# Kernel tuning notes

Measured on AMD Instinct MI355X. Metric: run time of the kernel, lower is better.

Reference implementation:

```python
import jax, jax.numpy as jnp
import numpy as np
import math

GAMMA = 0.97      # discounting
LAM = 0.95        # gae lambda
EPSILON = 0.3     # ppo clip
EPS = 0.2         # gpo clip (eps)
ENT_COST = 0.01
RSCALE = 1.0
ALPHA = 1.0
NUM_STEPS = 1.0e6 # normalization step count buffer


def _mlp(x, Ws, bs):
    for i, (W, b) in enumerate(zip(Ws, bs)):
        x = x @ W.T + b
        if i < len(Ws) - 1:
            x = jax.nn.silu(x)
    return x


def _dist_create(logits):
    loc, s = jnp.split(logits, 2, axis=-1)
    return loc, jax.nn.softplus(s) + 0.001


def _log_det_jac(x):
    # tanh bijector log|det J| per element
    return 2.0 * (math.log(2.0) - x - jax.nn.softplus(-2.0 * x))


def _log_prob(loc, scale, dist):
    lu = -0.5 * jnp.square((dist - loc) / scale)
    ln = 0.5 * math.log(2.0 * math.pi) + jnp.log(scale)
    return (lu - ln - _log_det_jac(dist)).sum(-1)


def _entropy(loc, scale, noise):
    ln = 0.5 * math.log(2.0 * math.pi) + jnp.log(scale)
    ent = (0.5 + ln) * jnp.ones_like(loc)
    dist = loc + scale * noise  # reparameterized sample (torch.normal)
    return (ent + _log_det_jac(dist)).sum(-1)


def _kl(pl, ps, ql, qs):
    vr = jnp.square(ps / qs)
    t1 = jnp.square((pl - ql) / qs)
    return (0.5 * (vr + t1 - 1.0 - jnp.log(vr))).mean(-1)


def _normalize(obs, rm, rv):
    var = jnp.clip(rv / (NUM_STEPS + 1.0), 1e-6, 1e6)
    return jnp.clip((obs - rm) / jnp.sqrt(var), -5.0, 5.0)


def _gae(truncation, termination, reward, values, bootstrap_value):
    tm = 1.0 - truncation
    v1 = jnp.concatenate([values[1:], bootstrap_value[None]], 0)
    deltas = (reward + GAMMA * (1.0 - termination) * v1 - values) * tm

    def step(acc, xs):
        d, te, tmask = xs
        acc = d + GAMMA * (1.0 - te) * tmask * LAM * acc
        return acc, acc

    _, vmx = jax.lax.scan(step, jnp.zeros_like(bootstrap_value),
                          (deltas, termination, tm), reverse=True)
    vs = vmx + values
    vs1 = jnp.concatenate([vs[1:], bootstrap_value[None]], 0)
    adv = (reward + GAMMA * (1.0 - termination) * vs1 - values) * tm
    return vs, adv


def _loss(observation, pobservation, reward, done, truncation, logits, action,
          noise, pw0, pb0, pw1, pb1, pw2, pb2, vw0, vb0, vw1, vb1, vw2, vb2,
          running_mean, running_variance, kl_coef):
    sg = jax.lax.stop_gradient
    Pw, Pb = [pw0, pw1, pw2], [pb0, pb1, pb2]
    Vw, Vb = [vw0, vw1, vw2], [vb0, vb1, vb2]

    obs_n = _normalize(observation, running_mean, running_variance)
    pobs_n = _normalize(pobservation, running_mean, running_variance)

    guider_logits = _mlp(obs_n[:-1], Pw, Pb)
    learner_logits = _mlp(pobs_n[:-1], Pw, Pb)
    baseline = _mlp(obs_n, Vw, Vb).squeeze(-1)  # [T+1, B]
    bootstrap = baseline[-1]
    baseline = baseline[:-1]

    reward_s = reward * RSCALE
    termination = done * (1.0 - truncation)

    loc, scale = _dist_create(logits)
    b_lp = _log_prob(loc, scale, action)
    gl, gs = _dist_create(guider_logits)
    g_lp = _log_prob(gl, gs, action)
    ll, ls = _dist_create(learner_logits)
    l_lp = _log_prob(ll, ls, action)

    kl_learner = _kl(sg(gl), sg(gs), ll, ls).mean()
    kl_guider = _kl(gl, gs, sg(ll), sg(ls))
    # use_clip = True branch
    diff = g_lp - l_lp
    m = jnp.where(diff > math.log(1.0 + EPS), 1.0,
                  jnp.where(diff < math.log(1.0 - EPS), 1.0, 0.0))
    kl_guider = (kl_guider * m).mean()

    vs, adv = _gae(truncation, termination, reward_s, sg(baseline), sg(bootstrap))
    vs = sg(vs)
    adv = sg((adv - adv.mean()) / (jnp.std(adv, ddof=1) + 1e-5))

    rho = jnp.exp(g_lp - b_lp)
    rho_clip = jnp.exp(jnp.clip(g_lp - sg(l_lp), math.log(1.0 - EPS), math.log(1.0 + EPS))
                       + sg(l_lp) - b_lp)
    rho_clip = jnp.clip(rho_clip, 1.0 - EPSILON, 1.0 + EPSILON)
    guider_policy_loss = -jnp.mean(jnp.minimum(rho * adv, rho_clip * adv))

    rho2 = jnp.exp(jnp.minimum(l_lp - b_lp, 10.0))  # stable_exp
    rho2c = jnp.clip(rho2, 1.0 - EPSILON, 1.0 + EPSILON)
    learner_policy_loss = -jnp.mean(jnp.minimum(rho2 * adv, rho2c * adv))

    v_err = vs - baseline
    v_loss = jnp.mean(v_err * v_err) * 0.25

    entropy = jnp.mean(_entropy(loc, scale, noise))
    entropy_loss = -ENT_COST * entropy

    learner_loss = kl_learner + learner_policy_loss * ALPHA  # use_clip
    guider_loss = kl_guider + guider_policy_loss
    total = learner_loss + guider_loss + v_loss + entropy_loss
    return total, guider_loss, learner_loss, kl_learner


def setup_inputs() -> dict:
    key = jax.random.key(0)
    T, B, OBS, ACT, H = 1024, 256, 64, 8, 256
    ks = iter(jax.random.split(key, 32))

    def lin(fin, fout):
        W = jax.random.normal(next(ks), (fout, fin), jnp.float32) / np.float32(np.sqrt(fin))
        b = jnp.zeros((fout,), jnp.float32)
        return W, b

    pw0, pb0 = lin(OBS, H); pw1, pb1 = lin(H, H); pw2, pb2 = lin(H, 2 * ACT)
    vw0, vb0 = lin(OBS, H); vw1, vb1 = lin(H, H); vw2, vb2 = lin(H, 1)

    observation = jax.random.normal(next(ks), (T + 1, B, OBS), jnp.float32)
    pobservation = observation + 0.1 * jax.random.normal(next(ks), (T + 1, B, OBS), jnp.float32)
    reward = jax.random.normal(next(ks), (T, B), jnp.float32)
    done = (jax.random.uniform(next(ks), (T, B)) < 0.01).astype(jnp.float32)
    truncation = (jax.random.uniform(next(ks), (T, B)) < 0.005).astype(jnp.float32)
    logits = 0.5 * jax.random.normal(next(ks), (T, B, 2 * ACT), jnp.float32)
    action = jax.random.normal(next(ks), (T, B, ACT), jnp.float32)
    noise = jax.random.normal(next(ks), (T, B, ACT), jnp.float32)
    running_mean = jnp.zeros((OBS,), jnp.float32)
    running_variance = jnp.ones((OBS,), jnp.float32) * NUM_STEPS  # unit variance after /num_steps
    kl_coef = jnp.ones((1,), jnp.float32)

    return {"observation": observation, "pobservation": pobservation,
            "reward": reward, "done": done, "truncation": truncation,
            "logits": logits, "action": action, "noise": noise,
            "pw0": pw0, "pb0": pb0, "pw1": pw1, "pb1": pb1, "pw2": pw2, "pb2": pb2,
            "vw0": vw0, "vb0": vb0, "vw1": vw1, "vb1": vb1, "vw2": vw2, "vb2": vb2,
            "running_mean": running_mean, "running_variance": running_variance,
            "kl_coef": kl_coef}


def reference(observation, pobservation, reward, done, truncation, logits, action,
              noise, pw0, pb0, pw1, pb1, pw2, pb2, vw0, vb0, vw1, vb1, vw2, vb2,
              running_mean, running_variance, kl_coef):
    return _loss(observation, pobservation, reward, done, truncation, logits,
                 action, noise, pw0, pb0, pw1, pb1, pw2, pb2, vw0, vb0, vw1, vb1,
                 vw2, vb2, running_mean, running_variance, kl_coef)
```

## Files before the change

### kernel.cpp

```cpp
#include <hip/hip_runtime.h>
#include <math.h>

#define GAMMA_   0.97f
#define LAM_     0.95f
#define EPSILON_ 0.3f
#define HLOG2PI_ 0.91893853320467274f
#define LOG2C_   0.69314718055994531f
#define LOG1P2_  0.18232155679395463f
#define LOG0P8_  (-0.22314355131420976f)

typedef unsigned short u16;
typedef unsigned int   u32;
typedef _Float16 half8 __attribute__((ext_vector_type(8)));
typedef _Float16 half4 __attribute__((ext_vector_type(4)));
typedef __attribute__((ext_vector_type(4))) float floatx4;
typedef __attribute__((ext_vector_type(8))) float floatx8;

constexpr int  TT     = 1024;
constexpr long ROWS_P = (long)TT * 256;
constexpr long ROWS_V = (long)(TT + 1) * 256;

constexpr long FR_W0P_HI = 0;
constexpr long FR_W0P_LO = 16384;
constexpr long FR_W1P_HI = 32768;
constexpr long FR_W1P_LO = 98304;
constexpr long FR_W2P_HI = 163840;
constexpr long FR_W2P_LO = 167936;
constexpr long FR_W0V_HI = 172032;
constexpr long FR_W0V_LO = 188416;
constexpr long FR_W1V_HI = 204800;
constexpr long FR_W1V_LO = 270336;
constexpr long FR_W2V_HI = 335872;
constexpr long FR_W2V_LO = 339968;
constexpr long FR_TOTAL  = 344064;

constexpr long WS_ACC  = 0;
constexpr long WS_INV  = 32;
constexpr long WS_ADV  = 96;
constexpr long WS_BASE = WS_ADV + ROWS_P;
constexpr long WS_GA   = WS_BASE + ROWS_V;
constexpr long WS_GP   = WS_GA + 8192;
constexpr long WS_BANK = WS_GP + 8192;


__device__ __forceinline__ float softplus_f(float x) {
  return (x > 20.f) ? x : log1pf(expf(x));
}
__device__ __forceinline__ float silu_f(float x) {
  return x * __builtin_amdgcn_rcpf(1.f + __expf(-x));
}
__device__ __forceinline__ float clamp30(float x) {
  return fminf(1e30f, fmaxf(-1e30f, x));
}

__global__ void convert_kernel(const float* __restrict__ pw0,
                               const float* __restrict__ pw1,
                               const float* __restrict__ pw2,
                               const float* __restrict__ vw0,
                               const float* __restrict__ vw1,
                               const float* __restrict__ vw2,
                               const float* __restrict__ rv,
                               float* __restrict__ inv_std,
                               float* __restrict__ accum,
                               float* __restrict__ accumB,
                               u16* __restrict__ frag) {
  if (blockIdx.x == 0) {
    int t = threadIdx.x;
    if (t < 32) accum[t] = 0.f;
    for (int i = t; i < 1024; i += 256) accumB[i] = 0.f;
    if (t < 64) {
      float var = rv[t] / 1000001.0f;
      var = fminf(1e6f, fmaxf(1e-6f, var));
      inv_std[t] = 1.f / sqrtf(var);
    }
  }
  int idx = blockIdx.x * 256 + threadIdx.x;
  const float* W; int kslog, K, nvalid; long hioff, looff; int e;
  if (idx < 16384)       { W = pw0; e = idx;          kslog = 1; K = 64;  nvalid = 256; hioff = FR_W0P_HI; looff = FR_W0P_LO; }
  else if (idx < 81920)  { W = pw1; e = idx - 16384;  kslog = 3; K = 256; nvalid = 256; hioff = FR_W1P_HI; looff = FR_W1P_LO; }
  else if (idx < 86016)  { W = pw2; e = idx - 81920;  kslog = 3; K = 256; nvalid = 16;  hioff = FR_W2P_HI; looff = FR_W2P_LO; }
  else if (idx < 102400) { W = vw0; e = idx - 86016;  kslog = 1; K = 64;  nvalid = 256; hioff = FR_W0V_HI; looff = FR_W0V_LO; }
  else if (idx < 167936) { W = vw1; e = idx - 102400; kslog = 3; K = 256; nvalid = 256; hioff = FR_W1V_HI; looff = FR_W1V_LO; }
  else                   { W = vw2; e = idx - 167936; kslog = 3; K = 256; nvalid = 1;   hioff = FR_W2V_HI; looff = FR_W2V_LO; }
  int j    = e & 7;
  int lane = (e >> 3) & 63;
  int ks   = (e >> 9) & ((1 << kslog) - 1);
  int nt   = e >> (9 + kslog);
  int n = nt * 16 + (lane & 15);
  int k = ks * 32 + ((lane >> 4) << 3) + j;
  float w = (n < nvalid) ? W[n * K + k] : 0.f;
  _Float16 hi = (_Float16)w;
  _Float16 lo = (_Float16)(w - (float)hi);
  frag[hioff + e] = *(u16*)&hi;
  frag[looff + e] = *(u16*)&lo;
}

constexpr int SX = 72;
constexpr int SH = 264;
constexpr int SO = 20;

__global__ __launch_bounds__(256, 3)
void policy_kernel(const float* __restrict__ obs,
                   const float* __restrict__ pobs,
                   const float* __restrict__ rm,
                   const float* __restrict__ inv_std,
                   const u16* __restrict__ frag,
                   const float* __restrict__ b0,
                   const float* __restrict__ b1,
                   const float* __restrict__ b2,
                   const float* __restrict__ logits,
                   const float* __restrict__ action,
                   const float* __restrict__ noise,
                   const float* __restrict__ adv,
                   const float* __restrict__ accum,
                   float* __restrict__ accumB) {
  __shared__ __align__(16) _Float16 H[64 * SH];
  __shared__ __align__(16) float OUTT[64 * SO];
  __shared__ float red[160];

  const int tid  = threadIdx.x;
  const long row0 = (long)blockIdx.x * 32;
  const int lane = tid & 63;
  const int wv   = tid >> 6;
  const int lm   = lane & 15;
  const int lq   = lane >> 4;

  _Float16* X = H;

  #pragma unroll
  for (int it = 0; it < 2; ++it) {
    int flat = it * 256 + tid;
    int vr = flat >> 3;
    int f0 = (flat & 7) * 8;
    const float* src = (vr < 32) ? obs : pobs;
    floatx8 v  = *(const floatx8*)&src[(row0 + (vr & 31)) * 64 + f0];
    floatx8 m  = *(const floatx8*)&rm[f0];
    floatx8 is = *(const floatx8*)&inv_std[f0];
    half8 h;
    #pragma unroll
    for (int j = 0; j < 8; ++j)
      h[j] = (_Float16)fminf(5.f, fmaxf(-5.f, (v[j] - m[j]) * is[j]));
    *(half8*)&X[vr * SX + f0] = h;
  }

  const int  er   = tid >> 3;
  const int  ed   = tid & 7;
  const long erow = row0 + er;
  float pf_a   = action[erow * 8 + ed];
  float pf_loc = logits[erow * 16 + ed];
  float pf_sr  = logits[erow * 16 + 8 + ed];
  float pf_nd  = noise[erow * 8 + ed];
  float pf_adv = adv[erow];
  float pf_s3  = accum[3];
  float pf_s4  = accum[4];

  const half8* B0h = (const half8*)(frag + FR_W0P_HI);
  const half8* B0l = (const half8*)(frag + FR_W0P_LO);
  half8 B0hr[2][4], B0lr[2][4];
  #pragma unroll
  for (int ks = 0; ks < 2; ++ks)
    #pragma unroll
    for (int nt = 0; nt < 4; ++nt) {
      int ntg = wv * 4 + nt;
      B0hr[ks][nt] = B0h[(ntg * 2 + ks) * 64 + lane];
      B0lr[ks][nt] = B0l[(ntg * 2 + ks) * 64 + lane];
    }

  floatx4 acc[4][4];
  #pragma unroll
  for (int nt = 0; nt < 4; ++nt) {
    floatx4 bz = *(const floatx4*)&b0[(wv * 4 + nt) * 16 + lq * 4];
    #pragma unroll
    for (int mt = 0; mt < 4; ++mt) acc[mt][nt] = bz;
  }
  __syncthreads();

  #pragma unroll
  for (int ks = 0; ks < 2; ++ks) {
    half8 A[4];
    #pragma unroll
    for (int mt = 0; mt < 4; ++mt)
      A[mt] = *(const half8*)&X[(mt * 16 + lm) * SX + ks * 32 + lq * 8];
    __builtin_amdgcn_s_setprio(1);
    #pragma unroll
    for (int mt = 0; mt < 4; ++mt)
      #pragma unroll
      for (int nt = 0; nt < 4; ++nt)
        acc[mt][nt] = __builtin_amdgcn_mfma_f32_16x16x32_f16(B0hr[ks][nt], A[mt], acc[mt][nt], 0, 0, 0);
    #pragma unroll
    for (int mt = 0; mt < 4; ++mt)
      #pragma unroll
      for (int nt = 0; nt < 4; ++nt)
        acc[mt][nt] = __builtin_amdgcn_mfma_f32_16x16x32_f16(B0lr[ks][nt], A[mt], acc[mt][nt], 0, 0, 0);
    __builtin_amdgcn_s_setprio(0);
  }

  const half8* B1h = (const half8*)(frag + FR_W1P_HI);
  const half8* B1l = (const half8*)(frag + FR_W1P_LO);
  half8 Bh[4], Bl[4], Bhn[4], Bln[4];
  #pragma unroll
  for (int nt = 0; nt < 4; ++nt) {
    int ntg = wv * 4 + nt;
    Bh[nt] = B1h[(ntg * 8) * 64 + lane];
    Bl[nt] = B1l[(ntg * 8) * 64 + lane];
  }

  __syncthreads();
  #pragma unroll
  for (int nt = 0; nt < 4; ++nt) {
    int colbase = (wv * 4 + nt) * 16 + lq * 4;
    #pragma unroll
    for (int mt = 0; mt < 4; ++mt) {
      int row = mt * 16 + lm;
      half4 h;
      #pragma unroll
      for (int reg = 0; reg < 4; ++reg)
        h[reg] = (_Float16)silu_f(acc[mt][nt][reg]);
      *(half4*)&H[row * SH + colbase] = h;
    }
  }
  #pragma unroll
  for (int nt = 0; nt < 4; ++nt) {
    floatx4 bz = *(const floatx4*)&b1[(wv * 4 + nt) * 16 + lq * 4];
    #pragma unroll
    for (int mt = 0; mt < 4; ++mt) acc[mt][nt] = bz;
  }
  __syncthreads();

  #pragma unroll 1
  for (int ks = 0; ks < 8; ++ks) {
    if (ks < 7) {
      #pragma unroll
      for (int nt = 0; nt < 4; ++nt) {
        int ntg = wv * 4 + nt;
        Bhn[nt] = B1h[(ntg * 8 + ks + 1) * 64 + lane];
        Bln[nt] = B1l[(ntg * 8 + ks + 1) * 64 + lane];
      }
    }
    half8 A[4];
    #pragma unroll
    for (int mt = 0; mt < 4; ++mt)
      A[mt] = *(const half8*)&H[(mt * 16 + lm) * SH + ks * 32 + lq * 8];
    __builtin_amdgcn_s_setprio(1);
    #pragma unroll
    for (int mt = 0; mt < 4; ++mt)
      #pragma unroll
      for (int nt = 0; nt < 4; ++nt)
        acc[mt][nt] = __builtin_amdgcn_mfma_f32_16x16x32_f16(Bh[nt], A[mt], acc[mt][nt], 0, 0, 0);
    #pragma unroll
    for (int mt = 0; mt < 4; ++mt)
      #pragma unroll
      for (int nt = 0; nt < 4; ++nt)
        acc[mt][nt] = __builtin_amdgcn_mfma_f32_16x16x32_f16(Bl[nt], A[mt], acc[mt][nt], 0, 0, 0);
    __builtin_amdgcn_s_setprio(0);
    if (ks < 7) {
      #pragma unroll
      for (int nt = 0; nt < 4; ++nt) { Bh[nt] = Bhn[nt]; Bl[nt] = Bln[nt]; }
    }
  }

  const half8* B2h = (const half8*)(frag + FR_W2P_HI);
  const half8* B2l = (const half8*)(frag + FR_W2P_LO);
  half8 B2hr[8], B2lr[8];
  #pragma unroll
  for (int ks = 0; ks < 8; ++ks) {
    B2hr[ks] = B2h[ks * 64 + lane];
    B2lr[ks] = B2l[ks * 64 + lane];
  }

  __syncthreads();
  #pragma unroll
  for (int nt = 0; nt < 4; ++nt) {
    int colbase = (wv * 4 + nt) * 16 + lq * 4;
    #pragma unroll
    for (int mt = 0; mt < 4; ++mt) {
      int row = mt * 16 + lm;
      half4 h;
      #pragma unroll
      for (int reg = 0; reg < 4; ++reg)
        h[reg] = (_Float16)silu_f(acc[mt][nt][reg]);
      *(half4*)&H[row * SH + colbase] = h;
    }
  }
  __syncthreads();

  {
    floatx4 c3a = (floatx4){0.f,0.f,0.f,0.f};
    floatx4 c3b = (floatx4){0.f,0.f,0.f,0.f};
    __builtin_amdgcn_s_setprio(1);
    #pragma unroll
    for (int ks = 0; ks < 8; ks += 2) {
      half8 A0 = *(const half8*)&H[(wv * 16 + lm) * SH + ks * 32 + lq * 8];
      half8 A1 = *(const half8*)&H[(wv * 16 + lm) * SH + (ks + 1) * 32 + lq * 8];
      c3a = __builtin_amdgcn_mfma_f32_16x16x32_f16(B2hr[ks],     A0, c3a, 0, 0, 0);
      c3b = __builtin_amdgcn_mfma_f32_16x16x32_f16(B2hr[ks + 1], A1, c3b, 0, 0, 0);
      c3a = __builtin_amdgcn_mfma_f32_16x16x32_f16(B2lr[ks],     A0, c3a, 0, 0, 0);
      c3b = __builtin_amdgcn_mfma_f32_16x16x32_f16(B2lr[ks + 1], A1, c3b, 0, 0, 0);
    }
    __builtin_amdgcn_s_setprio(0);
    floatx4 bias = *(const floatx4*)&b2[lq * 4];
    floatx4 o = c3a + c3b + bias;
    #pragma unroll
    for (int reg = 0; reg < 4; ++reg)
      OUTT[(wv * 16 + lm) * SO + lq * 4 + reg] = o[reg];
  }
  __syncthreads();

  {
    int r = er;
    int d = ed;

    float gl  = OUTT[r * SO + d];
    float gsr = OUTT[r * SO + 8 + d];
    float ll  = OUTT[(32 + r) * SO + d];
    float lsr = OUTT[(32 + r) * SO + 8 + d];
    float a   = pf_a;
    float loc = pf_loc;
    float sr  = pf_sr;
    float nd  = pf_nd;

    float gs = softplus_f(gsr) + 1e-3f;
    float ls = softplus_f(lsr) + 1e-3f;
    float sc = softplus_f(sr) + 1e-3f;
    float ldj = 2.f * (LOG2C_ - a - softplus_f(-2.f * a));
    float lgs = logf(gs), lls = logf(ls), lsc = logf(sc);
    float zg = (a - gl) / gs;
    float zl = (a - ll) / ls;
    float z  = (a - loc) / sc;
    float glp = -0.5f * zg * zg - lgs - HLOG2PI_ - ldj;
    float llp = -0.5f * zl * zl - lls - HLOG2PI_ - ldj;
    float blp = -0.5f * z * z - lsc - HLOG2PI_ - ldj;
    float ratio = gs / ls;
    float vr = ratio * ratio;
    float t1 = (gl - ll) / ls; t1 *= t1;
    float kl = 0.5f * (vr + t1 - 1.f) - (lgs - lls);
    float dist = loc + sc * nd;
    float ent = 0.5f + HLOG2PI_ + lsc
              + 2.f * (LOG2C_ - dist - softplus_f(-2.f * dist));

    #pragma unroll
    for (int o = 4; o > 0; o >>= 1) {
      glp += __shfl_down(glp, o, 8);
      llp += __shfl_down(llp, o, 8);
      blp += __shfl_down(blp, o, 8);
      kl  += __shfl_down(kl, o, 8);
      ent += __shfl_down(ent, o, 8);
    }

    if (d == 0) {
      kl *= 0.125f;
      kl  = clamp30(kl);
      ent = clamp30(ent);

      float diff = glp - llp;
      float m = (diff > LOG1P2_ || diff < LOG0P8_) ? 1.f : 0.f;

      float N = (float)ROWS_P;
      float sum = pf_s3, sumsq = pf_s4;
      float mean = sum / N;
      float var  = fmaxf((sumsq - sum * sum / N) / (N - 1.f), 0.f);
      float inv  = 1.f / (sqrtf(var) + 1e-5f);
      float a_n  = (pf_adv - mean) * inv;

      float rho = expf(fminf(glp - blp, 80.f));
      float cl  = fminf(LOG1P2_, fmaxf(LOG0P8_, diff));
      float rc  = expf(fminf(cl + llp - blp, 80.f));
      rc = fminf(1.f + EPSILON_, fmaxf(1.f - EPSILON_, rc));
      float gp = clamp30(fminf(rho * a_n, rc * a_n));

      float rho2 = expf(fminf(llp - blp, 10.f));
      float r2c  = fminf(1.f + EPSILON_, fmaxf(1.f - EPSILON_, rho2));
      float lp = clamp30(fminf(rho2 * a_n, r2c * a_n));

      red[r]       = kl;
      red[32 + r]  = kl * m;
      red[64 + r]  = ent;
      red[96 + r]  = gp;
      red[128 + r] = lp;
    }
  }
  __syncthreads();
  if (tid < 32) {
    float s0 = red[tid], s1 = red[32 + tid], s2 = red[64 + tid];
    float s3 = red[96 + tid], s4 = red[128 + tid];
    #pragma unroll
    for (int o = 16; o > 0; o >>= 1) {
      s0 += __shfl_down(s0, o, 32);
      s1 += __shfl_down(s1, o, 32);
      s2 += __shfl_down(s2, o, 32);
      s3 += __shfl_down(s3, o, 32);
      s4 += __shfl_down(s4, o, 32);
    }
    if (tid == 0) {
      float* bank = accumB + (blockIdx.x & 31) * 32;
      atomicAdd(&bank[0], s0);
      atomicAdd(&bank[1], s1);
      atomicAdd(&bank[2], s2);
      atomicAdd(&bank[6], s3);
      atomicAdd(&bank[7], s4);
    }
  }
}

__global__ __launch_bounds__(256, 3)
void value_kernel(const float* __restrict__ obs,
                  const float* __restrict__ rm,
                  const float* __restrict__ inv_std,
                  const u16* __restrict__ frag,
                  const float* __restrict__ b0,
                  const float* __restrict__ b1,
                  const float* __restrict__ b2,
                  float* __restrict__ baseline) {
  __shared__ __align__(16) _Float16 H[64 * SH];

  const int tid  = threadIdx.x;
  const long row0 = (long)blockIdx.x * 64;
  const int lane = tid & 63;
  const int wv   = tid >> 6;
  const int lm   = lane & 15;
  const int lq   = lane >> 4;

  _Float16* X = H;

  #pragma unroll
  for (int it = 0; it < 2; ++it) {
    int flat = it * 256 + tid;
    int vr = flat >> 3;
    int f0 = (flat & 7) * 8;
    floatx8 v  = *(const floatx8*)&obs[(row0 + vr) * 64 + f0];
    floatx8 m  = *(const floatx8*)&rm[f0];
    floatx8 is = *(const floatx8*)&inv_std[f0];
    half8 h;
    #pragma unroll
    for (int j = 0; j < 8; ++j)
      h[j] = (_Float16)fminf(5.f, fmaxf(-5.f, (v[j] - m[j]) * is[j]));
    *(half8*)&X[vr * SX + f0] = h;
  }

  const half8* B0h = (const half8*)(frag + FR_W0V_HI);
  const half8* B0l = (const half8*)(frag + FR_W0V_LO);
  half8 B0hr[2][4], B0lr[2][4];
  #pragma unroll
  for (int ks = 0; ks < 2; ++ks)
    #pragma unroll
    for (int nt = 0; nt < 4; ++nt) {
      int ntg = wv * 4 + nt;
      B0hr[ks][nt] = B0h[(ntg * 2 + ks) * 64 + lane];
      B0lr[ks][nt] = B0l[(ntg * 2 + ks) * 64 + lane];
    }

  floatx4 acc[4][4];
  #pragma unroll
  for (int nt = 0; nt < 4; ++nt) {
    floatx4 bz = *(const floatx4*)&b0[(wv * 4 + nt) * 16 + lq * 4];
    #pragma unroll
    for (int mt = 0; mt < 4; ++mt) acc[mt][nt] = bz;
  }
  __syncthreads();

  #pragma unroll
  for (int ks = 0; ks < 2; ++ks) {
    half8 A[4];
    #pragma unroll
    for (int mt = 0; mt < 4; ++mt)
      A[mt] = *(const half8*)&X[(mt * 16 + lm) * SX + ks * 32 + lq * 8];
    __builtin_amdgcn_s_setprio(1);
    #pragma unroll
    for (int mt = 0; mt < 4; ++mt)
      #pragma unroll
      for (int nt = 0; nt < 4; ++nt)
        acc[mt][nt] = __builtin_amdgcn_mfma_f32_16x16x32_f16(B0hr[ks][nt], A[mt], acc[mt][nt], 0, 0, 0);
    #pragma unroll
    for (int mt = 0; mt < 4; ++mt)
      #pragma unroll
      for (int nt = 0; nt < 4; ++nt)
        acc[mt][nt] = __builtin_amdgcn_mfma_f32_16x16x32_f16(B0lr[ks][nt], A[mt], acc[mt][nt], 0, 0, 0);
    __builtin_amdgcn_s_setprio(0);
  }

  const half8* B1h = (const half8*)(frag + FR_W1V_HI);
  const half8* B1l = (const half8*)(frag + FR_W1V_LO);
  half8 Bh[4], Bl[4], Bhn[4], Bln[4];
  #pragma unroll
  for (int nt = 0; nt < 4; ++nt) {
    int ntg = wv * 4 + nt;
    Bh[nt] = B1h[(ntg * 8) * 64 + lane];
    Bl[nt] = B1l[(ntg * 8) * 64 + lane];
  }

  __syncthreads();
  #pragma unroll
  for (int nt = 0; nt < 4; ++nt) {
    int colbase = (wv * 4 + nt) * 16 + lq * 4;
    #pragma unroll
    for (int mt = 0; mt < 4; ++mt) {
      int row = mt * 16 + lm;
      half4 h;
      #pragma unroll
      for (int reg = 0; reg < 4; ++reg)
        h[reg] = (_Float16)silu_f(acc[mt][nt][reg]);
      *(half4*)&H[row * SH + colbase] = h;
    }
  }
  #pragma unroll
  for (int nt = 0; nt < 4; ++nt) {
    floatx4 bz = *(const floatx4*)&b1[(wv * 4 + nt) * 16 + lq * 4];
    #pragma unroll
    for (int mt = 0; mt < 4; ++mt) acc[mt][nt] = bz;
  }
  __syncthreads();

  #pragma unroll 1
  for (int ks = 0; ks < 8; ++ks) {
    if (ks < 7) {
      #pragma unroll
      for (int nt = 0; nt < 4; ++nt) {
        int ntg = wv * 4 + nt;
        Bhn[nt] = B1h[(ntg * 8 + ks + 1) * 64 + lane];
        Bln[nt] = B1l[(ntg * 8 + ks + 1) * 64 + lane];
      }
    }
    half8 A[4];
    #pragma unroll
    for (int mt = 0; mt < 4; ++mt)
      A[mt] = *(const half8*)&H[(mt * 16 + lm) * SH + ks * 32 + lq * 8];
    __builtin_amdgcn_s_setprio(1);
    #pragma unroll
    for (int mt = 0; mt < 4; ++mt)
      #pragma unroll
      for (int nt = 0; nt < 4; ++nt)
        acc[mt][nt] = __builtin_amdgcn_mfma_f32_16x16x32_f16(Bh[nt], A[mt], acc[mt][nt], 0, 0, 0);
    #pragma unroll
    for (int mt = 0; mt < 4; ++mt)
      #pragma unroll
      for (int nt = 0; nt < 4; ++nt)
        acc[mt][nt] = __builtin_amdgcn_mfma_f32_16x16x32_f16(Bl[nt], A[mt], acc[mt][nt], 0, 0, 0);
    __builtin_amdgcn_s_setprio(0);
    if (ks < 7) {
      #pragma unroll
      for (int nt = 0; nt < 4; ++nt) { Bh[nt] = Bhn[nt]; Bl[nt] = Bln[nt]; }
    }
  }

  const half8* B2h = (const half8*)(frag + FR_W2V_HI);
  const half8* B2l = (const half8*)(frag + FR_W2V_LO);
  half8 B2hr[8], B2lr[8];
  #pragma unroll
  for (int ks = 0; ks < 8; ++ks) {
    B2hr[ks] = B2h[ks * 64 + lane];
    B2lr[ks] = B2l[ks * 64 + lane];
  }

  __syncthreads();
  #pragma unroll
  for (int nt = 0; nt < 4; ++nt) {
    int colbase = (wv * 4 + nt) * 16 + lq * 4;
    #pragma unroll
    for (int mt = 0; mt < 4; ++mt) {
      int row = mt * 16 + lm;
      half4 h;
      #pragma unroll
      for (int reg = 0; reg < 4; ++reg)
        h[reg] = (_Float16)silu_f(acc[mt][nt][reg]);
      *(half4*)&H[row * SH + colbase] = h;
    }
  }
  __syncthreads();

  {
    floatx4 c3a = (floatx4){0.f,0.f,0.f,0.f};
    floatx4 c3b = (floatx4){0.f,0.f,0.f,0.f};
    __builtin_amdgcn_s_setprio(1);
    #pragma unroll
    for (int ks = 0; ks < 8; ks += 2) {
      half8 A0 = *(const half8*)&H[(wv * 16 + lm) * SH + ks * 32 + lq * 8];
      half8 A1 = *(const half8*)&H[(wv * 16 + lm) * SH + (ks + 1) * 32 + lq * 8];
      c3a = __builtin_amdgcn_mfma_f32_16x16x32_f16(B2hr[ks],     A0, c3a, 0, 0, 0);
      c3b = __builtin_amdgcn_mfma_f32_16x16x32_f16(B2hr[ks + 1], A1, c3b, 0, 0, 0);
      c3a = __builtin_amdgcn_mfma_f32_16x16x32_f16(B2lr[ks],     A0, c3a, 0, 0, 0);
      c3b = __builtin_amdgcn_mfma_f32_16x16x32_f16(B2lr[ks + 1], A1, c3b, 0, 0, 0);
    }
    __builtin_amdgcn_s_setprio(0);
    if (lq == 0) baseline[row0 + wv * 16 + lm] = c3a[0] + c3b[0] + b2[0];
  }
}

__global__ void gae_phase1(const float* __restrict__ reward,
                           const float* __restrict__ done,
                           const float* __restrict__ trunc,
                           const float* __restrict__ baseline,
                           float* __restrict__ A, float* __restrict__ P) {
  int s = blockIdx.x, b = threadIdx.x;
  float Aa = 0.f, Pp = 1.f;
  for (int t = (s + 1) * 32 - 1; t >= s * 32; --t) {
    int idx = t * 256 + b;
    float r = reward[idx], d = done[idx], tr = trunc[idx];
    float tm = 1.f - tr;
    float te = d * tm;
    float bl = baseline[idx], bl1 = baseline[idx + 256];
    float g1 = GAMMA_ * (1.f - te);
    float delta = (r + g1 * bl1 - bl) * tm;
    float c = g1 * tm * LAM_;
    Aa = delta + c * Aa;
    Pp = c * Pp;
  }
  A[s * 256 + b] = Aa;
  P[s * 256 + b] = Pp;
}

__global__ void gae_phase3(const float* __restrict__ reward,
                           const float* __restrict__ done,
                           const float* __restrict__ trunc,
                           const float* __restrict__ baseline,
                           const float* __restrict__ A,
                           const float* __restrict__ P,
                           float* __restrict__ adv,
                           float* __restrict__ accum) {
  __shared__ float red[12];
  int s = blockIdx.x, b = threadIdx.x;
  float acc = 0.f;
  #pragma unroll 1
  for (int s2 = 31; s2 > s; --s2)
    acc = A[s2 * 256 + b] + P[s2 * 256 + b] * acc;
  int tend = (s + 1) * 32;
  float vnext = baseline[tend * 256 + b];
  float vs_next = acc + vnext;
  float sa = 0.f, sa2 = 0.f, sv2 = 0.f;
  for (int t = tend - 1; t >= s * 32; --t) {
    int idx = t * 256 + b;
    float r = reward[idx], d = done[idx], tr = trunc[idx];
    float tm = 1.f - tr;
    float te = d * tm;
    float bl = baseline[idx];
    float g1 = GAMMA_ * (1.f - te);
    float delta = (r + g1 * vnext - bl) * tm;
    acc = delta + g1 * tm * LAM_ * acc;
    float at = (r + g1 * vs_next - bl) * tm;
    at = fminf(1e15f, fmaxf(-1e15f, at));
    adv[idx] = at;
    sa += at; sa2 += at * at;
    sv2 += fminf(acc * acc, 1e30f);
    vs_next = acc + bl;
    vnext = bl;
  }
  float v0 = sa, v1 = sa2, v2 = sv2;
  #pragma unroll
  for (int o = 32; o > 0; o >>= 1) {
    v0 += __shfl_down(v0, o, 64);
    v1 += __shfl_down(v1, o, 64);
    v2 += __shfl_down(v2, o, 64);
  }
  int lane = threadIdx.x & 63, w = threadIdx.x >> 6;
  if (lane == 0) { red[w] = v0; red[4 + w] = v1; red[8 + w] = v2; }
  __syncthreads();
  if (threadIdx.x == 0) {
    float s0=0.f, s1=0.f, s2=0.f;
    for (int q = 0; q < 4; ++q) { s0 += red[q]; s1 += red[4+q]; s2 += red[8+q]; }
    atomicAdd(&accum[3], s0);
    atomicAdd(&accum[4], s1);
    atomicAdd(&accum[5], s2);
  }
}

__global__ void finalize_kernel(const float* __restrict__ accum,
                                const float* __restrict__ accumB,
                                float* __restrict__ out) {
  int t = threadIdx.x;
  float s0 = 0.f, s1 = 0.f, s2 = 0.f, s6 = 0.f, s7 = 0.f;
  if (t < 32) {
    const float* bank = accumB + t * 32;
    s0 = bank[0]; s1 = bank[1]; s2 = bank[2]; s6 = bank[6]; s7 = bank[7];
  }
  #pragma unroll
  for (int o = 16; o > 0; o >>= 1) {
    s0 += __shfl_down(s0, o, 64);
    s1 += __shfl_down(s1, o, 64);
    s2 += __shfl_down(s2, o, 64);
    s6 += __shfl_down(s6, o, 64);
    s7 += __shfl_down(s7, o, 64);
  }
  if (t == 0) {
    float N = (float)ROWS_P;
    float kl_learner = s0 / N;
    float kl_guider  = s1 / N;
    float entropy    = s2 / N;
    float v_loss     = 0.25f * accum[5] / N;
    float gp_loss    = -s6 / N;
    float lp_loss    = -s7 / N;
    float learner_loss = kl_learner + lp_loss;
    float guider_loss  = kl_guider + gp_loss;
    float total = learner_loss + guider_loss + v_loss - 0.01f * entropy;
    out[0] = total;
    out[1] = guider_loss;
    out[2] = learner_loss;
    out[3] = kl_learner;
  }
}

extern "C" void kernel_launch(void* const* d_in, const int* in_sizes, int n_in,
                              void* d_out, int out_size, void* d_ws, size_t ws_size,
                              hipStream_t stream) {
  (void)in_sizes; (void)n_in; (void)out_size; (void)ws_size;
  const float* obs    = (const float*)d_in[0];
  const float* pobs   = (const float*)d_in[1];
  const float* reward = (const float*)d_in[2];
  const float* done   = (const float*)d_in[3];
  const float* trunc  = (const float*)d_in[4];
  const float* logits = (const float*)d_in[5];
  const float* action = (const float*)d_in[6];
  const float* noise  = (const float*)d_in[7];
  const float* pw0 = (const float*)d_in[8];
  const float* pb0 = (const float*)d_in[9];
  const float* pw1 = (const float*)d_in[10];
  const float* pb1 = (const float*)d_in[11];
  const float* pw2 = (const float*)d_in[12];
  const float* pb2 = (const float*)d_in[13];
  const float* vw0 = (const float*)d_in[14];
  const float* vb0 = (const float*)d_in[15];
  const float* vw1 = (const float*)d_in[16];
  const float* vb1 = (const float*)d_in[17];
  const float* vw2 = (const float*)d_in[18];
  const float* vb2 = (const float*)d_in[19];
  const float* rm  = (const float*)d_in[20];
  const float* rv  = (const float*)d_in[21];

  u16*   frag  = (u16*)d_ws;
  float* fbase = (float*)d_ws + FR_TOTAL / 2;
  float* accum   = fbase + WS_ACC;
  float* inv_std = fbase + WS_INV;
  float* adv     = fbase + WS_ADV;
  float* base    = fbase + WS_BASE;
  float* gA      = fbase + WS_GA;
  float* gP      = fbase + WS_GP;
  float* accumB  = fbase + WS_BANK;
  float* out = (float*)d_out;

  convert_kernel<<<672, 256, 0, stream>>>(pw0, pw1, pw2, vw0, vw1, vw2,
                                          rv, inv_std, accum, accumB, frag);

  value_kernel<<<(int)(ROWS_V / 64), 256, 0, stream>>>(
      obs, rm, inv_std, frag, vb0, vb1, vb2, base);

  gae_phase1<<<32, 256, 0, stream>>>(reward, done, trunc, base, gA, gP);
  gae_phase3<<<32, 256, 0, stream>>>(reward, done, trunc, base, gA, gP,
                                     adv, accum);

  policy_kernel<<<(int)(ROWS_P / 32), 256, 0, stream>>>(
      obs, pobs, rm, inv_std, frag, pb0, pb1, pb2,
      logits, action, noise, adv, accum, accumB);

  finalize_kernel<<<1, 64, 0, stream>>>(accum, accumB, out);
}
```

Measured before the change: 509.6 us.

## Fuse policy and value MLP forwards into one kernel, defer advantage-dependent terms

Policy and value network forward passes are merged into a single launch with interleaved block roles (two policy blocks per value block), so the policy MLP no longer waits for the GAE scan. Per-row log-probs are written to workspace and a new epilogue kernel computes the advantage-dependent PPO terms after GAE, folding in the finalize step via a last-block counter. This removes the serialization between the value kernel, GAE and policy kernel and one launch. In exchange it adds extra global traffic for the three log-prob arrays, and the branchy fused kernel may raise register pressure.

```diff
diff --git a/kernel.cpp b/kernel.cpp
--- a/kernel.cpp
+++ b/kernel.cpp
@@ -41,6 +41,9 @@
 constexpr long WS_GA   = WS_BASE + ROWS_V;
 constexpr long WS_GP   = WS_GA + 8192;
 constexpr long WS_BANK = WS_GP + 8192;
+constexpr long WS_GLP  = WS_BANK + 1024;
+constexpr long WS_LLP  = WS_GLP + ROWS_P;
+constexpr long WS_BLP  = WS_LLP + ROWS_P;
 
 
 __device__ __forceinline__ float softplus_f(float x) {
@@ -100,488 +103,461 @@
 constexpr int SO = 20;
 
 __global__ __launch_bounds__(256, 3)
-void policy_kernel(const float* __restrict__ obs,
-                   const float* __restrict__ pobs,
-                   const float* __restrict__ rm,
-                   const float* __restrict__ inv_std,
-                   const u16* __restrict__ frag,
-                   const float* __restrict__ b0,
-                   const float* __restrict__ b1,
-                   const float* __restrict__ b2,
-                   const float* __restrict__ logits,
-                   const float* __restrict__ action,
-                   const float* __restrict__ noise,
-                   const float* __restrict__ adv,
-                   const float* __restrict__ accum,
-                   float* __restrict__ accumB) {
+void fused_fwd_kernel(const float* __restrict__ obs,
+                      const float* __restrict__ pobs,
+                      const float* __restrict__ rm,
+                      const float* __restrict__ inv_std,
+                      const u16* __restrict__ frag,
+                      const float* __restrict__ pb0,
+                      const float* __restrict__ pb1,
+                      const float* __restrict__ pb2,
+                      const float* __restrict__ vb0,
+                      const float* __restrict__ vb1,
+                      const float* __restrict__ vb2,
+                      const float* __restrict__ logits,
+                      const float* __restrict__ action,
+                      const float* __restrict__ noise,
+                      float* __restrict__ baseline,
+                      float* __restrict__ glpA,
+                      float* __restrict__ llpA,
+                      float* __restrict__ blpA,
+                      float* __restrict__ accumB) {
   __shared__ __align__(16) _Float16 H[64 * SH];
   __shared__ __align__(16) float OUTT[64 * SO];
-  __shared__ float red[160];
+  __shared__ float red[192];
 
   const int tid  = threadIdx.x;
-  const long row0 = (long)blockIdx.x * 32;
   const int lane = tid & 63;
   const int wv   = tid >> 6;
   const int lm   = lane & 15;
   const int lq   = lane >> 4;
 
+  int bid = blockIdx.x;
+  bool isP; long sub;
+  if (bid < 12288) {
+    int g = bid / 3, r = bid - g * 3;
+    if (r < 2) { isP = true;  sub = (long)g * 2 + r; }
+    else       { isP = false; sub = g; }
+  } else { isP = false; sub = 4096 + (bid - 12288); }
+
   _Float16* X = H;
 
-  #pragma unroll
-  for (int it = 0; it < 2; ++it) {
-    int flat = it * 256 + tid;
-    int vr = flat >> 3;
-    int f0 = (flat & 7) * 8;
-    const float* src = (vr < 32) ? obs : pobs;
-    floatx8 v  = *(const floatx8*)&src[(row0 + (vr & 31)) * 64 + f0];
-    floatx8 m  = *(const floatx8*)&rm[f0];
-    floatx8 is = *(const floatx8*)&inv_std[f0];
-    half8 h;
-    #pragma unroll
-    for (int j = 0; j < 8; ++j)
-      h[j] = (_Float16)fminf(5.f, fmaxf(-5.f, (v[j] - m[j]) * is[j]));
-    *(half8*)&X[vr * SX + f0] = h;
-  }
-
-  const int  er   = tid >> 3;
-  const int  ed   = tid & 7;
-  const long erow = row0 + er;
-  float pf_a   = action[erow * 8 + ed];
-  float pf_loc = logits[erow * 16 + ed];
-  float pf_sr  = logits[erow * 16 + 8 + ed];
-  float pf_nd  = noise[erow * 8 + ed];
-  float pf_adv = adv[erow];
-  float pf_s3  = accum[3];
-  float pf_s4  = accum[4];
-
-  const half8* B0h = (const half8*)(frag + FR_W0P_HI);
-  const half8* B0l = (const half8*)(frag + FR_W0P_LO);
-  half8 B0hr[2][4], B0lr[2][4];
-  #pragma unroll
-  for (int ks = 0; ks < 2; ++ks)
-    #pragma unroll
-    for (int nt = 0; nt < 4; ++nt) {
-      int ntg = wv * 4 + nt;
-      B0hr[ks][nt] = B0h[(ntg * 2 + ks) * 64 + lane];
-      B0lr[ks][nt] = B0l[(ntg * 2 + ks) * 64 + lane];
-    }
-
-  floatx4 acc[4][4];
-  #pragma unroll
-  for (int nt = 0; nt < 4; ++nt) {
-    floatx4 bz = *(const floatx4*)&b0[(wv * 4 + nt) * 16 + lq * 4];
-    #pragma unroll
-    for (int mt = 0; mt < 4; ++mt) acc[mt][nt] = bz;
-  }
-  __syncthreads();
-
-  #pragma unroll
-  for (int ks = 0; ks < 2; ++ks) {
-    half8 A[4];
-    #pragma unroll
-    for (int mt = 0; mt < 4; ++mt)
-      A[mt] = *(const half8*)&X[(mt * 16 + lm) * SX + ks * 32 + lq * 8];
-    __builtin_amdgcn_s_setprio(1);
-    #pragma unroll
-    for (int mt = 0; mt < 4; ++mt)
-      #pragma unroll
-      for (int nt = 0; nt < 4; ++nt)
-        acc[mt][nt] = __builtin_amdgcn_mfma_f32_16x16x32_f16(B0hr[ks][nt], A[mt], acc[mt][nt], 0, 0, 0);
-    #pragma unroll
-    for (int mt = 0; mt < 4; ++mt)
-      #pragma unroll
-      for (int nt = 0; nt < 4; ++nt)
-        acc[mt][nt] = __builtin_amdgcn_mfma_f32_16x16x32_f16(B0lr[ks][nt], A[mt], acc[mt][nt], 0, 0, 0);
-    __builtin_amdgcn_s_setprio(0);
-  }
-
-  const half8* B1h = (const half8*)(frag + FR_W1P_HI);
-  const half8* B1l = (const half8*)(frag + FR_W1P_LO);
-  half8 Bh[4], Bl[4], Bhn[4], Bln[4];
-  #pragma unroll
-  for (int nt = 0; nt < 4; ++nt) {
-    int ntg = wv * 4 + nt;
-    Bh[nt] = B1h[(ntg * 8) * 64 + lane];
-    Bl[nt] = B1l[(ntg * 8) * 64 + lane];
-  }
-
-  __syncthreads();
-  #pragma unroll
-  for (int nt = 0; nt < 4; ++nt) {
-    int colbase = (wv * 4 + nt) * 16 + lq * 4;
-    #pragma unroll
-    for (int mt = 0; mt < 4; ++mt) {
-      int row = mt * 16 + lm;
-      half4 h;
-      #pragma unroll
-      for (int reg = 0; reg < 4; ++reg)
-        h[reg] = (_Float16)silu_f(acc[mt][nt][reg]);
-      *(half4*)&H[row * SH + colbase] = h;
-    }
-  }
-  #pragma unroll
-  for (int nt = 0; nt < 4; ++nt) {
-    floatx4 bz = *(const floatx4*)&b1[(wv * 4 + nt) * 16 + lq * 4];
-    #pragma unroll
-    for (int mt = 0; mt < 4; ++mt) acc[mt][nt] = bz;
-  }
-  __syncthreads();
-
-  #pragma unroll 1
-  for (int ks = 0; ks < 8; ++ks) {
-    if (ks < 7) {
+  if (isP) {
+    const long row0 = sub * 32;
+    #pragma unroll
+    for (int it = 0; it < 2; ++it) {
+      int flat = it * 256 + tid;
+      int vr = flat >> 3;
+      int f0 = (flat & 7) * 8;
+      const float* src = (vr < 32) ? obs : pobs;
+      floatx8 v  = *(const floatx8*)&src[(row0 + (vr & 31)) * 64 + f0];
+      floatx8 m  = *(const floatx8*)&rm[f0];
+      floatx8 is = *(const floatx8*)&inv_std[f0];
+      half8 h;
+      #pragma unroll
+      for (int j = 0; j < 8; ++j)
+        h[j] = (_Float16)fminf(5.f, fmaxf(-5.f, (v[j] - m[j]) * is[j]));
+      *(half8*)&X[vr * SX + f0] = h;
+    }
+
+    const int  er   = tid >> 3;
+    const int  ed   = tid & 7;
+    const long erow = row0 + er;
+    float pf_a   = action[erow * 8 + ed];
+    float pf_loc = logits[erow * 16 + ed];
+    float pf_sr  = logits[erow * 16 + 8 + ed];
+    float pf_nd  = noise[erow * 8 + ed];
+
+    const half8* B0h = (const half8*)(frag + FR_W0P_HI);
+    const half8* B0l = (const half8*)(frag + FR_W0P_LO);
+    half8 B0hr[2][4], B0lr[2][4];
+    #pragma unroll
+    for (int ks = 0; ks < 2; ++ks)
       #pragma unroll
       for (int nt = 0; nt < 4; ++nt) {
         int ntg = wv * 4 + nt;
-        Bhn[nt] = B1h[(ntg * 8 + ks + 1) * 64 + lane];
-        Bln[nt] = B1l[(ntg * 8 + ks + 1) * 64 + lane];
-      }
-    }
-    half8 A[4];
-    #pragma unroll
-    for (int mt = 0; mt < 4; ++mt)
-      A[mt] = *(const half8*)&H[(mt * 16 + lm) * SH + ks * 32 + lq * 8];
-    __builtin_amdgcn_s_setprio(1);
-    #pragma unroll
-    for (int mt = 0; mt < 4; ++mt)
-      #pragma unroll
-      for (int nt = 0; nt < 4; ++nt)
-        acc[mt][nt] = __builtin_amdgcn_mfma_f32_16x16x32_f16(Bh[nt], A[mt], acc[mt][nt], 0, 0, 0);
-    #pragma unroll
-    for (int mt = 0; mt < 4; ++mt)
-      #pragma unroll
-      for (int nt = 0; nt < 4; ++nt)
-        acc[mt][nt] = __builtin_amdgcn_mfma_f32_16x16x32_f16(Bl[nt], A[mt], acc[mt][nt], 0, 0, 0);
-    __builtin_amdgcn_s_setprio(0);
-    if (ks < 7) {
-      #pragma unroll
-      for (int nt = 0; nt < 4; ++nt) { Bh[nt] = Bhn[nt]; Bl[nt] = Bln[nt]; }
-    }
-  }
-
-  const half8* B2h = (const half8*)(frag + FR_W2P_HI);
-  const half8* B2l = (const half8*)(frag + FR_W2P_LO);
-  half8 B2hr[8], B2lr[8];
-  #pragma unroll
-  for (int ks = 0; ks < 8; ++ks) {
-    B2hr[ks] = B2h[ks * 64 + lane];
-    B2lr[ks] = B2l[ks * 64 + lane];
-  }
-
-  __syncthreads();
-  #pragma unroll
-  for (int nt = 0; nt < 4; ++nt) {
-    int colbase = (wv * 4 + nt) * 16 + lq * 4;
-    #pragma unroll
-    for (int mt = 0; mt < 4; ++mt) {
-      int row = mt * 16 + lm;
-      half4 h;
+        B0hr[ks][nt] = B0h[(ntg * 2 + ks) * 64 + lane];
+        B0lr[ks][nt] = B0l[(ntg * 2 + ks) * 64 + lane];
+      }
+
+    floatx4 acc[4][4];
+    #pragma unroll
+    for (int nt = 0; nt < 4; ++nt) {
+      floatx4 bz = *(const floatx4*)&pb0[(wv * 4 + nt) * 16 + lq * 4];
+      #pragma unroll
+      for (int mt = 0; mt < 4; ++mt) acc[mt][nt] = bz;
+    }
+    __syncthreads();
+
+    #pragma unroll
+    for (int ks = 0; ks < 2; ++ks) {
+      half8 A[4];
+      #pragma unroll
+      for (int mt = 0; mt < 4; ++mt)
+        A[mt] = *(const half8*)&X[(mt * 16 + lm) * SX + ks * 32 + lq * 8];
+      __builtin_amdgcn_s_setprio(1);
+      #pragma unroll
+      for (int mt = 0; mt < 4; ++mt)
+        #pragma unroll
+        for (int nt = 0; nt < 4; ++nt)
+          acc[mt][nt] = __builtin_amdgcn_mfma_f32_16x16x32_f16(B0hr[ks][nt], A[mt], acc[mt][nt], 0, 0, 0);
+      #pragma unroll
+      for (int mt = 0; mt < 4; ++mt)
+        #pragma unroll
+        for (int nt = 0; nt < 4; ++nt)
+          acc[mt][nt] = __builtin_amdgcn_mfma_f32_16x16x32_f16(B0lr[ks][nt], A[mt], acc[mt][nt], 0, 0, 0);
+      __builtin_amdgcn_s_setprio(0);
+    }
+
+    const half8* B1h = (const half8*)(frag + FR_W1P_HI);
+    const half8* B1l = (const half8*)(frag + FR_W1P_LO);
+    half8 Bh[4], Bl[4], Bhn[4], Bln[4];
+    #pragma unroll
+    for (int nt = 0; nt < 4; ++nt) {
+      int ntg = wv * 4 + nt;
+      Bh[nt] = B1h[(ntg * 8) * 64 + lane];
+      Bl[nt] = B1l[(ntg * 8) * 64 + lane];
+    }
+
+    __syncthreads();
+    #pragma unroll
+    for (int nt = 0; nt < 4; ++nt) {
+      int colbase = (wv * 4 + nt) * 16 + lq * 4;
+      #pragma unroll
+      for (int mt = 0; mt < 4; ++mt) {
+        int row = mt * 16 + lm;
+        half4 h;
+        #pragma unroll
+        for (int reg = 0; reg < 4; ++reg)
+          h[reg] = (_Float16)silu_f(acc[mt][nt][reg]);
+        *(half4*)&H[row * SH + colbase] = h;
+      }
+    }
+    #pragma unroll
+    for (int nt = 0; nt < 4; ++nt) {
+      floatx4 bz = *(const floatx4*)&pb1[(wv * 4 + nt) * 16 + lq * 4];
+      #pragma unroll
+      for (int mt = 0; mt < 4; ++mt) acc[mt][nt] = bz;
+    }
+    __syncthreads();
+
+    #pragma unroll 1
+    for (int ks = 0; ks < 8; ++ks) {
+      if (ks < 7) {
+        #pragma unroll
+        for (int nt = 0; nt < 4; ++nt) {
+          int ntg = wv * 4 + nt;
+          Bhn[nt] = B1h[(ntg * 8 + ks + 1) * 64 + lane];
+          Bln[nt] = B1l[(ntg * 8 + ks + 1) * 64 + lane];
+        }
+      }
+      half8 A[4];
+      #pragma unroll
+      for (int mt = 0; mt < 4; ++mt)
+        A[mt] = *(const half8*)&H[(mt * 16 + lm) * SH + ks * 32 + lq * 8];
+      __builtin_amdgcn_s_setprio(1);
+      #pragma unroll
+      for (int mt = 0; mt < 4; ++mt)
+        #pragma unroll
+        for (int nt = 0; nt < 4; ++nt)
+          acc[mt][nt] = __builtin_amdgcn_mfma_f32_16x16x32_f16(Bh[nt], A[mt], acc[mt][nt], 0, 0, 0);
+      #pragma unroll
+      for (int mt = 0; mt < 4; ++mt)
+        #pragma unroll
+        for (int nt = 0; nt < 4; ++nt)
+          acc[mt][nt] = __builtin_amdgcn_mfma_f32_16x16x32_f16(Bl[nt], A[mt], acc[mt][nt], 0, 0, 0);
+      __builtin_amdgcn_s_setprio(0);
+      if (ks < 7) {
+        #pragma unroll
+        for (int nt = 0; nt < 4; ++nt) { Bh[nt] = Bhn[nt]; Bl[nt] = Bln[nt]; }
+      }
+    }
+
+    const half8* B2h = (const half8*)(frag + FR_W2P_HI);
+    const half8* B2l = (const half8*)(frag + FR_W2P_LO);
+    half8 B2hr[8], B2lr[8];
+    #pragma unroll
+    for (int ks = 0; ks < 8; ++ks) {
+      B2hr[ks] = B2h[ks * 64 + lane];
+      B2lr[ks] = B2l[ks * 64 + lane];
+    }
+
+    __syncthreads();
+    #pragma unroll
+    for (int nt = 0; nt < 4; ++nt) {
+      int colbase = (wv * 4 + nt) * 16 + lq * 4;
+      #pragma unroll
+      for (int mt = 0; mt < 4; ++mt) {
+        int row = mt * 16 + lm;
+        half4 h;
+        #pragma unroll
+        for (int reg = 0; reg < 4; ++reg)
+          h[reg] = (_Float16)silu_f(acc[mt][nt][reg]);
+        *(half4*)&H[row * SH + colbase] = h;
+      }
+    }
+    __syncthreads();
+
+    {
+      floatx4 c3a = (floatx4){0.f,0.f,0.f,0.f};
+      floatx4 c3b = (floatx4){0.f,0.f,0.f,0.f};
+      __builtin_amdgcn_s_setprio(1);
+      #pragma unroll
+      for (int ks = 0; ks < 8; ks += 2) {
+        half8 A0 = *(const half8*)&H[(wv * 16 + lm) * SH + ks * 32 + lq * 8];
+        half8 A1 = *(const half8*)&H[(wv * 16 + lm) * SH + (ks + 1) * 32 + lq * 8];
+        c3a = __builtin_amdgcn_mfma_f32_16x16x32_f16(B2hr[ks],     A0, c3a, 0, 0, 0);
+        c3b = __builtin_amdgcn_mfma_f32_16x16x32_f16(B2hr[ks + 1], A1, c3b, 0, 0, 0);
+        c3a = __builtin_amdgcn_mfma_f32_16x16x32_f16(B2lr[ks],     A0, c3a, 0, 0, 0);
+        c3b = __builtin_amdgcn_mfma_f32_16x16x32_f16(B2lr[ks + 1], A1, c3b, 0, 0, 0);
+      }
+      __builtin_amdgcn_s_setprio(0);
+      floatx4 bias = *(const floatx4*)&pb2[lq * 4];
+      floatx4 o = c3a + c3b + bias;
       #pragma unroll
       for (int reg = 0; reg < 4; ++reg)
-        h[reg] = (_Float16)silu_f(acc[mt][nt][reg]);
-      *(half4*)&H[row * SH + colbase] = h;
-    }
-  }
-  __syncthreads();
-
-  {
-    floatx4 c3a = (floatx4){0.f,0.f,0.f,0.f};
-    floatx4 c3b = (floatx4){0.f,0.f,0.f,0.f};
-    __builtin_amdgcn_s_setprio(1);
-    #pragma unroll
-    for (int ks = 0; ks < 8; ks += 2) {
-      half8 A0 = *(const half8*)&H[(wv * 16 + lm) * SH + ks * 32 + lq * 8];
-      half8 A1 = *(const half8*)&H[(wv * 16 + lm) * SH + (ks + 1) * 32 + lq * 8];
-      c3a = __builtin_amdgcn_mfma_f32_16x16x32_f16(B2hr[ks],     A0, c3a, 0, 0, 0);
-      c3b = __builtin_amdgcn_mfma_f32_16x16x32_f16(B2hr[ks + 1], A1, c3b, 0, 0, 0);
-      c3a = __builtin_amdgcn_mfma_f32_16x16x32_f16(B2lr[ks],     A0, c3a, 0, 0, 0);
-      c3b = __builtin_amdgcn_mfma_f32_16x16x32_f16(B2lr[ks + 1], A1, c3b, 0, 0, 0);
-    }
-    __builtin_amdgcn_s_setprio(0);
-    floatx4 bias = *(const floatx4*)&b2[lq * 4];
-    floatx4 o = c3a + c3b + bias;
-    #pragma unroll
-    for (int reg = 0; reg < 4; ++reg)
-      OUTT[(wv * 16 + lm) * SO + lq * 4 + reg] = o[reg];
-  }
-  __syncthreads();
-
-  {
-    int r = er;
-    int d = ed;
-
-    float gl  = OUTT[r * SO + d];
-    float gsr = OUTT[r * SO + 8 + d];
-    float ll  = OUTT[(32 + r) * SO + d];
-    float lsr = OUTT[(32 + r) * SO + 8 + d];
-    float a   = pf_a;
-    float loc = pf_loc;
-    float sr  = pf_sr;
-    float nd  = pf_nd;
-
-    float gs = softplus_f(gsr) + 1e-3f;
-    float ls = softplus_f(lsr) + 1e-3f;
-    float sc = softplus_f(sr) + 1e-3f;
-    float ldj = 2.f * (LOG2C_ - a - softplus_f(-2.f * a));
-    float lgs = logf(gs), lls = logf(ls), lsc = logf(sc);
-    float zg = (a - gl) / gs;
-    float zl = (a - ll) / ls;
-    float z  = (a - loc) / sc;
-    float glp = -0.5f * zg * zg - lgs - HLOG2PI_ - ldj;
-    float llp = -0.5f * zl * zl - lls - HLOG2PI_ - ldj;
-    float blp = -0.5f * z * z - lsc - HLOG2PI_ - ldj;
-    float ratio = gs / ls;
-    float vr = ratio * ratio;
-    float t1 = (gl - ll) / ls; t1 *= t1;
-    float kl = 0.5f * (vr + t1 - 1.f) - (lgs - lls);
-    float dist = loc + sc * nd;
-    float ent = 0.5f + HLOG2PI_ + lsc
-              + 2.f * (LOG2C_ - dist - softplus_f(-2.f * dist));
-
-    #pragma unroll
-    for (int o = 4; o > 0; o >>= 1) {
-      glp += __shfl_down(glp, o, 8);
-      llp += __shfl_down(llp, o, 8);
-      blp += __shfl_down(blp, o, 8);
-      kl  += __shfl_down(kl, o, 8);
-      ent += __shfl_down(ent, o, 8);
-    }
-
-    if (d == 0) {
-      kl *= 0.125f;
-      kl  = clamp30(kl);
-      ent = clamp30(ent);
-
-      float diff = glp - llp;
-      float m = (diff > LOG1P2_ || diff < LOG0P8_) ? 1.f : 0.f;
-
-      float N = (float)ROWS_P;
-      float sum = pf_s3, sumsq = pf_s4;
-      float mean = sum / N;
-      float var  = fmaxf((sumsq - sum * sum / N) / (N - 1.f), 0.f);
-      float inv  = 1.f / (sqrtf(var) + 1e-5f);
-      float a_n  = (pf_adv - mean) * inv;
-
-      float rho = expf(fminf(glp - blp, 80.f));
-      float cl  = fminf(LOG1P2_, fmaxf(LOG0P8_, diff));
-      float rc  = expf(fminf(cl + llp - blp, 80.f));
-      rc = fminf(1.f + EPSILON_, fmaxf(1.f - EPSILON_, rc));
-      float gp = clamp30(fminf(rho * a_n, rc * a_n));
-
-      float rho2 = expf(fminf(llp - blp, 10.f));
-      float r2c  = fminf(1.f + EPSILON_, fmaxf(1.f - EPSILON_, rho2));
-      float lp = clamp30(fminf(rho2 * a_n, r2c * a_n));
-
-      red[r]       = kl;
-      red[32 + r]  = kl * m;
-      red[64 + r]  = ent;
-      red[96 + r]  = gp;
-      red[128 + r] = lp;
-    }
-  }
-  __syncthreads();
-  if (tid < 32) {
-    float s0 = red[tid], s1 = red[32 + tid], s2 = red[64 + tid];
-    float s3 = red[96 + tid], s4 = red[128 + tid];
-    #pragma unroll
-    for (int o = 16; o > 0; o >>= 1) {
-      s0 += __shfl_down(s0, o, 32);
-      s1 += __shfl_down(s1, o, 32);
-      s2 += __shfl_down(s2, o, 32);
-      s3 += __shfl_down(s3, o, 32);
-      s4 += __shfl_down(s4, o, 32);
-    }
-    if (tid == 0) {
-      float* bank = accumB + (blockIdx.x & 31) * 32;
-      atomicAdd(&bank[0], s0);
-      atomicAdd(&bank[1], s1);
-      atomicAdd(&bank[2], s2);
-      atomicAdd(&bank[6], s3);
-      atomicAdd(&bank[7], s4);
-    }
-  }
-}
-
-__global__ __launch_bounds__(256, 3)
-void value_kernel(const float* __restrict__ obs,
-                  const float* __restrict__ rm,
-                  const float* __restrict__ inv_std,
-                  const u16* __restrict__ frag,
-                  const float* __restrict__ b0,
-                  const float* __restrict__ b1,
-                  const float* __restrict__ b2,
-                  float* __restrict__ baseline) {
-  __shared__ __align__(16) _Float16 H[64 * SH];
-
-  const int tid  = threadIdx.x;
-  const long row0 = (long)blockIdx.x * 64;
-  const int lane = tid & 63;
-  const int wv   = tid >> 6;
-  const int lm   = lane & 15;
-  const int lq   = lane >> 4;
-
-  _Float16* X = H;
-
-  #pragma unroll
-  for (int it = 0; it < 2; ++it) {
-    int flat = it * 256 + tid;
-    int vr = flat >> 3;
-    int f0 = (flat & 7) * 8;
-    floatx8 v  = *(const floatx8*)&obs[(row0 + vr) * 64 + f0];
-    floatx8 m  = *(const floatx8*)&rm[f0];
-    floatx8 is = *(const floatx8*)&inv_std[f0];
-    half8 h;
-    #pragma unroll
-    for (int j = 0; j < 8; ++j)
-      h[j] = (_Float16)fminf(5.f, fmaxf(-5.f, (v[j] - m[j]) * is[j]));
-    *(half8*)&X[vr * SX + f0] = h;
-  }
-
-  const half8* B0h = (const half8*)(frag + FR_W0V_HI);
-  const half8* B0l = (const half8*)(frag + FR_W0V_LO);
-  half8 B0hr[2][4], B0lr[2][4];
-  #pragma unroll
-  for (int ks = 0; ks < 2; ++ks)
-    #pragma unroll
-    for (int nt = 0; nt < 4; ++nt) {
-      int ntg = wv * 4 + nt;
-      B0hr[ks][nt] = B0h[(ntg * 2 + ks) * 64 + lane];
-      B0lr[ks][nt] = B0l[(ntg * 2 + ks) * 64 + lane];
-    }
-
-  floatx4 acc[4][4];
-  #pragma unroll
-  for (int nt = 0; nt < 4; ++nt) {
-    floatx4 bz = *(const floatx4*)&b0[(wv * 4 + nt) * 16 + lq * 4];
-    #pragma unroll
-    for (int mt = 0; mt < 4; ++mt) acc[mt][nt] = bz;
-  }
-  __syncthreads();
-
-  #pragma unroll
-  for (int ks = 0; ks < 2; ++ks) {
-    half8 A[4];
-    #pragma unroll
-    for (int mt = 0; mt < 4; ++mt)
-      A[mt] = *(const half8*)&X[(mt * 16 + lm) * SX + ks * 32 + lq * 8];
-    __builtin_amdgcn_s_setprio(1);
-    #pragma unroll
-    for (int mt = 0; mt < 4; ++mt)
-      #pragma unroll
-      for (int nt = 0; nt < 4; ++nt)
-        acc[mt][nt] = __builtin_amdgcn_mfma_f32_16x16x32_f16(B0hr[ks][nt], A[mt], acc[mt][nt], 0, 0, 0);
-    #pragma unroll
-    for (int mt = 0; mt < 4; ++mt)
-      #pragma unroll
-      for (int nt = 0; nt < 4; ++nt)
-        acc[mt][nt] = __builtin_amdgcn_mfma_f32_16x16x32_f16(B0lr[ks][nt], A[mt], acc[mt][nt], 0, 0, 0);
-    __builtin_amdgcn_s_setprio(0);
-  }
-
-  const half8* B1h = (const half8*)(frag + FR_W1V_HI);
-  const half8* B1l = (const half8*)(frag + FR_W1V_LO);
-  half8 Bh[4], Bl[4], Bhn[4], Bln[4];
-  #pragma unroll
-  for (int nt = 0; nt < 4; ++nt) {
-    int ntg = wv * 4 + nt;
-    Bh[nt] = B1h[(ntg * 8) * 64 + lane];
-    Bl[nt] = B1l[(ntg * 8) * 64 + lane];
-  }
-
-  __syncthreads();
-  #pragma unroll
-  for (int nt = 0; nt < 4; ++nt) {
-    int colbase = (wv * 4 + nt) * 16 + lq * 4;
-    #pragma unroll
-    for (int mt = 0; mt < 4; ++mt) {
-      int row = mt * 16 + lm;
-      half4 h;
-      #pragma unroll
-      for (int reg = 0; reg < 4; ++reg)
-        h[reg] = (_Float16)silu_f(acc[mt][nt][reg]);
-      *(half4*)&H[row * SH + colbase] = h;
-    }
-  }
-  #pragma unroll
-  for (int nt = 0; nt < 4; ++nt) {
-    floatx4 bz = *(const floatx4*)&b1[(wv * 4 + nt) * 16 + lq * 4];
-    #pragma unroll
-    for (int mt = 0; mt < 4; ++mt) acc[mt][nt] = bz;
-  }
-  __syncthreads();
-
-  #pragma unroll 1
-  for (int ks = 0; ks < 8; ++ks) {
-    if (ks < 7) {
+        OUTT[(wv * 16 + lm) * SO + lq * 4 + reg] = o[reg];
+    }
+    __syncthreads();
+
+    {
+      int r = er, d = ed;
+      float gl  = OUTT[r * SO + d];
+      float gsr = OUTT[r * SO + 8 + d];
+      float ll  = OUTT[(32 + r) * SO + d];
+      float lsr = OUTT[(32 + r) * SO + 8 + d];
+      float a   = pf_a;
+      float loc = pf_loc;
+      float sr  = pf_sr;
+      float nd  = pf_nd;
+
+      float gs = softplus_f(gsr) + 1e-3f;
+      float ls = softplus_f(lsr) + 1e-3f;
+      float sc = softplus_f(sr) + 1e-3f;
+      float ldj = 2.f * (LOG2C_ - a - softplus_f(-2.f * a));
+      float lgs = logf(gs), lls = logf(ls), lsc = logf(sc);
+      float zg = (a - gl) / gs;
+      float zl = (a - ll) / ls;
+      float z  = (a - loc) / sc;
+      float glp = -0.5f * zg * zg - lgs - HLOG2PI_ - ldj;
+      float llp = -0.5f * zl * zl - lls - HLOG2PI_ - ldj;
+      float blp = -0.5f * z * z - lsc - HLOG2PI_ - ldj;
+      float ratio = gs / ls;
+      float vr = ratio * ratio;
+      float t1 = (gl - ll) / ls; t1 *= t1;
+      float kl = 0.5f * (vr + t1 - 1.f) - (lgs - lls);
+      float dist = loc + sc * nd;
+      float ent = 0.5f + HLOG2PI_ + lsc
+                + 2.f * (LOG2C_ - dist - softplus_f(-2.f * dist));
+
+      #pragma unroll
+      for (int o = 4; o > 0; o >>= 1) {
+        glp += __shfl_down(glp, o, 8);
+        llp += __shfl_down(llp, o, 8);
+        blp += __shfl_down(blp, o, 8);
+        kl  += __shfl_down(kl, o, 8);
+        ent += __shfl_down(ent, o, 8);
+      }
+
+      if (d == 0) {
+        kl *= 0.125f;
+        kl  = clamp30(kl);
+        ent = clamp30(ent);
+        float diff = glp - llp;
+        float m = (diff > LOG1P2_ || diff < LOG0P8_) ? 1.f : 0.f;
+        red[r]        = kl;
+        red[32 + r]   = kl * m;
+        red[64 + r]   = ent;
+        red[96 + r]   = glp;
+        red[128 + r]  = llp;
+        red[160 + r]  = blp;
+      }
+    }
+    __syncthreads();
+    if (tid < 96) {
+      int a = tid >> 5, i = tid & 31;
+      float v = red[96 + tid];
+      float* dst = (a == 0) ? glpA : (a == 1) ? llpA : blpA;
+      dst[row0 + i] = v;
+    }
+    if (tid < 32) {
+      float s0 = red[tid], s1 = red[32 + tid], s2 = red[64 + tid];
+      #pragma unroll
+      for (int o = 16; o > 0; o >>= 1) {
+        s0 += __shfl_down(s0, o, 32);
+        s1 += __shfl_down(s1, o, 32);
+        s2 += __shfl_down(s2, o, 32);
+      }
+      if (tid == 0) {
+        float* bank = accumB + (bid & 31) * 32;
+        atomicAdd(&bank[0], s0);
+        atomicAdd(&bank[1], s1);
+        atomicAdd(&bank[2], s2);
+      }
+    }
+  } else {
+    const long row0 = sub * 64;
+    #pragma unroll
+    for (int it = 0; it < 2; ++it) {
+      int flat = it * 256 + tid;
+      int vr = flat >> 3;
+      int f0 = (flat & 7) * 8;
+      floatx8 v  = *(const floatx8*)&obs[(row0 + vr) * 64 + f0];
+      floatx8 m  = *(const floatx8*)&rm[f0];
+      floatx8 is = *(const floatx8*)&inv_std[f0];
+      half8 h;
+      #pragma unroll
+      for (int j = 0; j < 8; ++j)
+        h[j] = (_Float16)fminf(5.f, fmaxf(-5.f, (v[j] - m[j]) * is[j]));
+      *(half8*)&X[vr * SX + f0] = h;
+    }
+
+    const half8* B0h = (const half8*)(frag + FR_W0V_HI);
+    const half8* B0l = (const half8*)(frag + FR_W0V_LO);
+    half8 B0hr[2][4], B0lr[2][4];
+    #pragma unroll
+    for (int ks = 0; ks < 2; ++ks)
       #pragma unroll
       for (int nt = 0; nt < 4; ++nt) {
         int ntg = wv * 4 + nt;
-        Bhn[nt] = B1h[(ntg * 8 + ks + 1) * 64 + lane];
-        Bln[nt] = B1l[(ntg * 8 + ks + 1) * 64 + lane];
-      }
-    }
-    half8 A[4];
-    #pragma unroll
-    for (int mt = 0; mt < 4; ++mt)
-      A[mt] = *(const half8*)&H[(mt * 16 + lm) * SH + ks * 32 + lq * 8];
-    __builtin_amdgcn_s_setprio(1);
-    #pragma unroll
-    for (int mt = 0; mt < 4; ++mt)
-      #pragma unroll
-      for (int nt = 0; nt < 4; ++nt)
-        acc[mt][nt] = __builtin_amdgcn_mfma_f32_16x16x32_f16(Bh[nt], A[mt], acc[mt][nt], 0, 0, 0);
-    #pragma unroll
-    for (int mt = 0; mt < 4; ++mt)
-      #pragma unroll
-      for (int nt = 0; nt < 4; ++nt)
-        acc[mt][nt] = __builtin_amdgcn_mfma_f32_16x16x32_f16(Bl[nt], A[mt], acc[mt][nt], 0, 0, 0);
-    __builtin_amdgcn_s_setprio(0);
-    if (ks < 7) {
-      #pragma unroll
-      for (int nt = 0; nt < 4; ++nt) { Bh[nt] = Bhn[nt]; Bl[nt] = Bln[nt]; }
-    }
-  }
-
-  const half8* B2h = (const half8*)(frag + FR_W2V_HI);
-  const half8* B2l = (const half8*)(frag + FR_W2V_LO);
-  half8 B2hr[8], B2lr[8];
-  #pragma unroll
-  for (int ks = 0; ks < 8; ++ks) {
-    B2hr[ks] = B2h[ks * 64 + lane];
-    B2lr[ks] = B2l[ks * 64 + lane];
-  }
-
-  __syncthreads();
-  #pragma unroll
-  for (int nt = 0; nt < 4; ++nt) {
-    int colbase = (wv * 4 + nt) * 16 + lq * 4;
-    #pragma unroll
-    for (int mt = 0; mt < 4; ++mt) {
-      int row = mt * 16 + lm;
-      half4 h;
-      #pragma unroll
-      for (int reg = 0; reg < 4; ++reg)
-        h[reg] = (_Float16)silu_f(acc[mt][nt][reg]);
-      *(half4*)&H[row * SH + colbase] = h;
-    }
-  }
-  __syncthreads();
-
-  {
-    floatx4 c3a = (floatx4){0.f,0.f,0.f,0.f};
-    floatx4 c3b = (floatx4){0.f,0.f,0.f,0.f};
-    __builtin_amdgcn_s_setprio(1);
-    #pragma unroll
-    for (int ks = 0; ks < 8; ks += 2) {
-      half8 A0 = *(const half8*)&H[(wv * 16 + lm) * SH + ks * 32 + lq * 8];
-      half8 A1 = *(const half8*)&H[(wv * 16 + lm) * SH + (ks + 1) * 32 + lq * 8];
-      c3a = __builtin_amdgcn_mfma_f32_16x16x32_f16(B2hr[ks],     A0, c3a, 0, 0, 0);
-      c3b = __builtin_amdgcn_mfma_f32_16x16x32_f16(B2hr[ks + 1], A1, c3b, 0, 0, 0);
-      c3a = __builtin_amdgcn_mfma_f32_16x16x32_f16(B2lr[ks],     A0, c3a, 0, 0, 0);
-      c3b = __builtin_amdgcn_mfma_f32_16x16x32_f16(B2lr[ks + 1], A1, c3b, 0, 0, 0);
-    }
-    __builtin_amdgcn_s_setprio(0);
-    if (lq == 0) baseline[row0 + wv * 16 + lm] = c3a[0] + c3b[0] + b2[0];
+        B0hr[ks][nt] = B0h[(ntg * 2 + ks) * 64 + lane];
+        B0lr[ks][nt] = B0l[(ntg * 2 + ks) * 64 + lane];
+      }
+
+    floatx4 acc[4][4];
+    #pragma unroll
+    for (int nt = 0; nt < 4; ++nt) {
+      floatx4 bz = *(const floatx4*)&vb0[(wv * 4 + nt) * 16 + lq * 4];
+      #pragma unroll
+      for (int mt = 0; mt < 4; ++mt) acc[mt][nt] = bz;
+    }
+    __syncthreads();
+
+    #pragma unroll
+    for (int ks = 0; ks < 2; ++ks) {
+      half8 A[4];
+      #pragma unroll
+      for (int mt = 0; mt < 4; ++mt)
+        A[mt] = *(const half8*)&X[(mt * 16 + lm) * SX + ks * 32 + lq * 8];
+      __builtin_amdgcn_s_setprio(1);
+      #pragma unroll
+      for (int mt = 0; mt < 4; ++mt)
+        #pragma unroll
+        for (int nt = 0; nt < 4; ++nt)
+          acc[mt][nt] = __builtin_amdgcn_mfma_f32_16x16x32_f16(B0hr[ks][nt], A[mt], acc[mt][nt], 0, 0, 0);
+      #pragma unroll
+      for (int mt = 0; mt < 4; ++mt)
+        #pragma unroll
+        for (int nt = 0; nt < 4; ++nt)
+          acc[mt][nt] = __builtin_amdgcn_mfma_f32_16x16x32_f16(B0lr[ks][nt], A[mt], acc[mt][nt], 0, 0, 0);
+      __builtin_amdgcn_s_setprio(0);
+    }
+
+    const half8* B1h = (const half8*)(frag + FR_W1V_HI);
+    const half8* B1l = (const half8*)(frag + FR_W1V_LO);
+    half8 Bh[4], Bl[4], Bhn[4], Bln[4];
+    #pragma unroll
+    for (int nt = 0; nt < 4; ++nt) {
+      int ntg = wv * 4 + nt;
+      Bh[nt] = B1h[(ntg * 8) * 64 + lane];
+      Bl[nt] = B1l[(ntg * 8) * 64 + lane];
+    }
+
+    __syncthreads();
+    #pragma unroll
+    for (int nt = 0; nt < 4; ++nt) {
+      int colbase = (wv * 4 + nt) * 16 + lq * 4;
+      #pragma unroll
+      for (int mt = 0; mt < 4; ++mt) {
+        int row = mt * 16 + lm;
+        half4 h;
+        #pragma unroll
+        for (int reg = 0; reg < 4; ++reg)
+          h[reg] = (_Float16)silu_f(acc[mt][nt][reg]);
+        *(half4*)&H[row * SH + colbase] = h;
+      }
+    }
+    #pragma unroll
+    for (int nt = 0; nt < 4; ++nt) {
+      floatx4 bz = *(const floatx4*)&vb1[(wv * 4 + nt) * 16 + lq * 4];
+      #pragma unroll
+      for (int mt = 0; mt < 4; ++mt) acc[mt][nt] = bz;
+    }
+    __syncthreads();
+
+    #pragma unroll 1
+    for (int ks = 0; ks < 8; ++ks) {
+      if (ks < 7) {
+        #pragma unroll
+        for (int nt = 0; nt < 4; ++nt) {
+          int ntg = wv * 4 + nt;
+          Bhn[nt] = B1h[(ntg * 8 + ks + 1) * 64 + lane];
+          Bln[nt] = B1l[(ntg * 8 + ks + 1) * 64 + lane];
+        }
+      }
+      half8 A[4];
+      #pragma unroll
+      for (int mt = 0; mt < 4; ++mt)
+        A[mt] = *(const half8*)&H[(mt * 16 + lm) * SH + ks * 32 + lq * 8];
+      __builtin_amdgcn_s_setprio(1);
+      #pragma unroll
+      for (int mt = 0; mt < 4; ++mt)
+        #pragma unroll
+        for (int nt = 0; nt < 4; ++nt)
+          acc[mt][nt] = __builtin_amdgcn_mfma_f32_16x16x32_f16(Bh[nt], A[mt], acc[mt][nt], 0, 0, 0);
+      #pragma unroll
+      for (int mt = 0; mt < 4; ++mt)
+        #pragma unroll
+        for (int nt = 0; nt < 4; ++nt)
+          acc[mt][nt] = __builtin_amdgcn_mfma_f32_16x16x32_f16(Bl[nt], A[mt], acc[mt][nt], 0, 0, 0);
+      __builtin_amdgcn_s_setprio(0);
+      if (ks < 7) {
+        #pragma unroll
+        for (int nt = 0; nt < 4; ++nt) { Bh[nt] = Bhn[nt]; Bl[nt] = Bln[nt]; }
+      }
+    }
+
+    const half8* B2h = (const half8*)(frag + FR_W2V_HI);
+    const half8* B2l = (const half8*)(frag + FR_W2V_LO);
+    half8 B2hr[8], B2lr[8];
+    #pragma unroll
+    for (int ks = 0; ks < 8; ++ks) {
+      B2hr[ks] = B2h[ks * 64 + lane];
+      B2lr[ks] = B2l[ks * 64 + lane];
+    }
+
+    __syncthreads();
+    #pragma unroll
+    for (int nt = 0; nt < 4; ++nt) {
+      int colbase = (wv * 4 + nt) * 16 + lq * 4;
+      #pragma unroll
+      for (int mt = 0; mt < 4; ++mt) {
+        int row = mt * 16 + lm;
+        half4 h;
+        #pragma unroll
+        for (int reg = 0; reg < 4; ++reg)
+          h[reg] = (_Float16)silu_f(acc[mt][nt][reg]);
+        *(half4*)&H[row * SH + colbase] = h;
+      }
+    }
+    __syncthreads();
+
+    {
+      floatx4 c3a = (floatx4){0.f,0.f,0.f,0.f};
+      floatx4 c3b = (floatx4){0.f,0.f,0.f,0.f};
+      __builtin_amdgcn_s_setprio(1);
+      #pragma unroll
+      for (int ks = 0; ks < 8; ks += 2) {
+        half8 A0 = *(const half8*)&H[(wv * 16 + lm) * SH + ks * 32 + lq * 8];
+        half8 A1 = *(const half8*)&H[(wv * 16 + lm) * SH + (ks + 1) * 32 + lq * 8];
+        c3a = __builtin_amdgcn_mfma_f32_16x16x32_f16(B2hr[ks],     A0, c3a, 0, 0, 0);
+        c3b = __builtin_amdgcn_mfma_f32_16x16x32_f16(B2hr[ks + 1], A1, c3b, 0, 0, 0);
+        c3a = __builtin_amdgcn_mfma_f32_16x16x32_f16(B2lr[ks],     A0, c3a, 0, 0, 0);
+        c3b = __builtin_amdgcn_mfma_f32_16x16x32_f16(B2lr[ks + 1], A1, c3b, 0, 0, 0);
+      }
+      __builtin_amdgcn_s_setprio(0);
+      if (lq == 0) baseline[row0 + wv * 16 + lm] = c3a[0] + c3b[0] + vb2[0];
+    }
   }
 }
 
@@ -662,38 +638,90 @@
   }
 }
 
-__global__ void finalize_kernel(const float* __restrict__ accum,
-                                const float* __restrict__ accumB,
-                                float* __restrict__ out) {
-  int t = threadIdx.x;
-  float s0 = 0.f, s1 = 0.f, s2 = 0.f, s6 = 0.f, s7 = 0.f;
-  if (t < 32) {
-    const float* bank = accumB + t * 32;
-    s0 = bank[0]; s1 = bank[1]; s2 = bank[2]; s6 = bank[6]; s7 = bank[7];
-  }
+__global__ __launch_bounds__(256)
+void epi2_kernel(const float* __restrict__ glpA,
+                 const float* __restrict__ llpA,
+                 const float* __restrict__ blpA,
+                 const float* __restrict__ adv,
+                 float* __restrict__ accum,
+                 float* __restrict__ accumB,
+                 float* __restrict__ out) {
+  __shared__ float red2[8];
+  __shared__ int lastFlag;
+  int tid = threadIdx.x;
+  long row = (long)blockIdx.x * 256 + tid;
+
+  float glp = glpA[row], llp = llpA[row], blp = blpA[row], av = adv[row];
+  float N = (float)ROWS_P;
+  float sum = accum[3], sumsq = accum[4];
+  float mean = sum / N;
+  float var  = fmaxf((sumsq - sum * sum / N) / (N - 1.f), 0.f);
+  float inv  = 1.f / (sqrtf(var) + 1e-5f);
+  float a_n  = (av - mean) * inv;
+
+  float diff = glp - llp;
+  float rho = expf(fminf(glp - blp, 80.f));
+  float cl  = fminf(LOG1P2_, fmaxf(LOG0P8_, diff));
+  float rc  = expf(fminf(cl + llp - blp, 80.f));
+  rc = fminf(1.f + EPSILON_, fmaxf(1.f - EPSILON_, rc));
+  float gp = clamp30(fminf(rho * a_n, rc * a_n));
+
+  float rho2 = expf(fminf(llp - blp, 10.f));
+  float r2c  = fminf(1.f + EPSILON_, fmaxf(1.f - EPSILON_, rho2));
+  float lp = clamp30(fminf(rho2 * a_n, r2c * a_n));
+
   #pragma unroll
-  for (int o = 16; o > 0; o >>= 1) {
-    s0 += __shfl_down(s0, o, 64);
-    s1 += __shfl_down(s1, o, 64);
-    s2 += __shfl_down(s2, o, 64);
-    s6 += __shfl_down(s6, o, 64);
-    s7 += __shfl_down(s7, o, 64);
-  }
-  if (t == 0) {
-    float N = (float)ROWS_P;
-    float kl_learner = s0 / N;
-    float kl_guider  = s1 / N;
-    float entropy    = s2 / N;
-    float v_loss     = 0.25f * accum[5] / N;
-    float gp_loss    = -s6 / N;
-    float lp_loss    = -s7 / N;
-    float learner_loss = kl_learner + lp_loss;
-    float guider_loss  = kl_guider + gp_loss;
-    float total = learner_loss + guider_loss + v_loss - 0.01f * entropy;
-    out[0] = total;
-    out[1] = guider_loss;
-    out[2] = learner_loss;
-    out[3] = kl_learner;
+  for (int o = 32; o > 0; o >>= 1) {
+    gp += __shfl_down(gp, o, 64);
+    lp += __shfl_down(lp, o, 64);
+  }
+  int lane = tid & 63, w = tid >> 6;
+  if (lane == 0) { red2[w] = gp; red2[4 + w] = lp; }
+  __syncthreads();
+  if (tid == 0) {
+    float sg = 0.f, sl = 0.f;
+    for (int q = 0; q < 4; ++q) { sg += red2[q]; sl += red2[4 + q]; }
+    float* bank = accumB + (blockIdx.x & 31) * 32;
+    atomicAdd(&bank[6], sg);
+    atomicAdd(&bank[7], sl);
+    __threadfence();
+    u32 old = atomicAdd((u32*)&accum[24], 1u);
+    lastFlag = (old == (u32)(gridDim.x - 1)) ? 1 : 0;
+  }
+  __syncthreads();
+  if (lastFlag) {
+    float s0 = 0.f, s1 = 0.f, s2 = 0.f, s6 = 0.f, s7 = 0.f;
+    if (tid < 32) {
+      float* bank = accumB + tid * 32;
+      s0 = atomicAdd(&bank[0], 0.f);
+      s1 = atomicAdd(&bank[1], 0.f);
+      s2 = atomicAdd(&bank[2], 0.f);
+      s6 = atomicAdd(&bank[6], 0.f);
+      s7 = atomicAdd(&bank[7], 0.f);
+    }
+    #pragma unroll
+    for (int o = 16; o > 0; o >>= 1) {
+      s0 += __shfl_down(s0, o, 32);
+      s1 += __shfl_down(s1, o, 32);
+      s2 += __shfl_down(s2, o, 32);
+      s6 += __shfl_down(s6, o, 32);
+      s7 += __shfl_down(s7, o, 32);
+    }
+    if (tid == 0) {
+      float kl_learner = s0 / N;
+      float kl_guider  = s1 / N;
+      float entropy    = s2 / N;
+      float v_loss     = 0.25f * accum[5] / N;
+      float gp_loss    = -s6 / N;
+      float lp_loss    = -s7 / N;
+      float learner_loss = kl_learner + lp_loss;
+      float guider_loss  = kl_guider + gp_loss;
+      float total = learner_loss + guider_loss + v_loss - 0.01f * entropy;
+      out[0] = total;
+      out[1] = guider_loss;
+      out[2] = learner_loss;
+      out[3] = kl_learner;
+    }
   }
 }
 
@@ -733,21 +761,22 @@
   float* gA      = fbase + WS_GA;
   float* gP      = fbase + WS_GP;
   float* accumB  = fbase + WS_BANK;
+  float* glpA    = fbase + WS_GLP;
+  float* llpA    = fbase + WS_LLP;
+  float* blpA    = fbase + WS_BLP;
   float* out = (float*)d_out;
 
   convert_kernel<<<672, 256, 0, stream>>>(pw0, pw1, pw2, vw0, vw1, vw2,
                                           rv, inv_std, accum, accumB, frag);
 
-  value_kernel<<<(int)(ROWS_V / 64), 256, 0, stream>>>(
-      obs, rm, inv_std, frag, vb0, vb1, vb2, base);
+  fused_fwd_kernel<<<12292, 256, 0, stream>>>(
+      obs, pobs, rm, inv_std, frag, pb0, pb1, pb2, vb0, vb1, vb2,
+      logits, action, noise, base, glpA, llpA, blpA, accumB);
 
   gae_phase1<<<32, 256, 0, stream>>>(reward, done, trunc, base, gA, gP);
   gae_phase3<<<32, 256, 0, stream>>>(reward, done, trunc, base, gA, gP,
                                      adv, accum);
 
-  policy_kernel<<<(int)(ROWS_P / 32), 256, 0, stream>>>(
-      obs, pobs, rm, inv_std, frag, pb0, pb1, pb2,
-      logits, action, noise, adv, accum, accumB);
-
-  finalize_kernel<<<1, 64, 0, stream>>>(accum, accumB, out);
-}
+  epi2_kernel<<<1024, 256, 0, stream>>>(glpA, llpA, blpA, adv,
+                                        accum, accumB, out);
+}
```

Result: slower. 523.9 us (+2.8%).
